# Performance work log

Hardware: AMD Instinct MI355X
Metric: run time of the kernel (lower is better)

## Reference

```python
import jax, jax.numpy as jnp
import numpy as np

DEPTH = 18                      # perfect binary tree depth -> N = 2**DEPTH - 1 nodes
N_NODES = 2 ** DEPTH - 1        # 262143
VOCAB, E, H = 2048, 64, 64


def setup_inputs() -> dict:
    key = jax.random.key(0)
    ks = jax.random.split(key, 10)
    token_ids = jax.random.randint(ks[0], (N_NODES,), 0, VOCAB, dtype=jnp.int32)
    emb = jax.random.normal(ks[1], (VOCAB, E), dtype=jnp.float32)
    emb = emb.at[0].set(0.0)  # padding_idx=0 row is zero in torch
    s = 0.1  # keep gates out of hard saturation
    return {
        "token_ids": token_ids,
        "emb": emb,
        "W_iou": jax.random.normal(ks[2], (3 * H, E), dtype=jnp.float32) * s,
        "b_Wiou": jnp.zeros((3 * H,), dtype=jnp.float32),
        "U_iou": jax.random.normal(ks[3], (3 * H, 2 * H), dtype=jnp.float32) * s,
        "b_Uiou": jnp.zeros((3 * H,), dtype=jnp.float32),
        "W_f": jax.random.normal(ks[4], (2 * H, E), dtype=jnp.float32) * s,
        "b_Wf": jnp.zeros((2 * H,), dtype=jnp.float32),
        "U_f": jax.random.normal(ks[5], (2 * H, 2 * H), dtype=jnp.float32) * s,
        "b_Uf": jnp.zeros((2 * H,), dtype=jnp.float32),
        "depth": DEPTH,
    }


def _tree_lstm(token_ids, emb, W_iou, b_Wiou, U_iou, b_Uiou, W_f, b_Wf, U_f, b_Uf, depth):
    """Level-synchronous bottom-up Binary TreeLSTM over a perfect binary tree.

    Node i has children 2i+1 (left), 2i+2 (right); level l occupies
    indices [2**l - 1, 2**(l+1) - 2]. Children of level-l node k sit at
    offsets 2k, 2k+1 of level l+1, so a reshape gives (left, right) pairs.
    """
    Hd = W_f.shape[0] // 2
    h = c = None
    for l in range(depth - 1, -1, -1):
        start, n = 2 ** l - 1, 2 ** l
        x = emb[token_ids[start:start + n]]                    # [n, E]
        if h is None:  # leaves: zero left/right states (both children zero)
            h_cat = jnp.zeros((n, 2 * Hd), dtype=x.dtype)
            c_lr = jnp.zeros((n, 2, Hd), dtype=x.dtype)
        else:
            h_cat = h.reshape(n, 2 * Hd)                        # [h_l | h_r]
            c_lr = c.reshape(n, 2, Hd)
        iou = jax.nn.sigmoid(x @ W_iou.T + b_Wiou + h_cat @ U_iou.T + b_Uiou)
        i_g, o_g, u_g = jnp.split(iou, 3, axis=1)
        u_g = jnp.tanh(u_g)  # faithful: tanh(sigmoid(u_pre)) as in the source
        f = jax.nn.sigmoid(x @ W_f.T + b_Wf + h_cat @ U_f.T + b_Uf)
        f_l, f_r = f[:, :Hd], f[:, Hd:]
        c = i_g * u_g + f_l * c_lr[:, 0] + f_r * c_lr[:, 1]
        h = o_g * jnp.tanh(c)
    return jnp.stack([h, c])  # [2, 1, H]: root (h, c)


def reference(token_ids, emb, W_iou, b_Wiou, U_iou, b_Uiou, W_f, b_Wf, U_f, b_Uf, depth):
    return _tree_lstm(token_ids, emb, W_iou, b_Wiou, U_iou, b_Uiou,
                      W_f, b_Wf, U_f, b_Uf, depth)
```

## Files before the change

kernel.cpp:

```cpp
#include <hip/hip_runtime.h>

typedef __bf16 bf16;
typedef __bf16 bf16x8 __attribute__((ext_vector_type(8)));
typedef float f32x4 __attribute__((ext_vector_type(4)));

#define DEPTH   18
#define N_NODES ((1 << DEPTH) - 1)
#define KDIM    192
#define RDIM    320
#define A_PAD   200
#define LOG2E   1.4426950408889634f

__device__ __forceinline__ float rcpf(float x) { return __builtin_amdgcn_rcpf(x); }
__device__ __forceinline__ float sig2(float p)  { return rcpf(1.f + exp2f(-p)); }
__device__ __forceinline__ float tanhf_(float x){ return 2.f * rcpf(1.f + exp2f(-2.f * LOG2E * x)) - 1.f; }

__device__ __forceinline__ void gates(const f32x4* acc,
        const float4& bI, const float4& bO, const float4& bU,
        const float4& bL, const float4& bR,
        const float4& cl, const float4& cr, float4& c4, float4& h4) {
    const float* pbI = &bI.x; const float* pbO = &bO.x; const float* pbU = &bU.x;
    const float* pbL = &bL.x; const float* pbR = &bR.x;
    const float* pcl = &cl.x; const float* pcr = &cr.x;
    float* pc4 = &c4.x; float* ph4 = &h4.x;
#pragma unroll
    for (int r = 0; r < 4; r++) {
        float i_g = sig2(acc[0][r] + pbI[r]);
        float o_g = sig2(acc[1][r] + pbO[r]);
        float u_g = tanhf_(sig2(acc[2][r] + pbU[r]));
        float fl  = sig2(acc[3][r] + pbL[r]);
        float fr  = sig2(acc[4][r] + pbR[r]);
        float c = i_g * u_g + fl * pcl[r] + fr * pcr[r];
        pc4[r] = c;
        ph4[r] = o_g * tanhf_(c);
    }
}

__global__ void prep_all(const float* __restrict__ emb,
                     const float* __restrict__ W_iou, const float* __restrict__ U_iou,
                     const float* __restrict__ W_f,   const float* __restrict__ U_f,
                     const float* __restrict__ b_Wiou, const float* __restrict__ b_Uiou,
                     const float* __restrict__ b_Wf,   const float* __restrict__ b_Uf,
                     bf16* __restrict__ Wcat, float* __restrict__ bias, bf16* __restrict__ emb16,
                     bf16* __restrict__ leafH, float* __restrict__ leafC) {
    __shared__ __align__(16) bf16 Wl[192 * 72];
    __shared__ __align__(16) bf16 Al[64 * 72];
    const int blk = blockIdx.x, tid = threadIdx.x;
    if (blk < 512) {
        int t = blk * 256 + tid;
        emb16[t] = (bf16)emb[t];
        if (t < RDIM * KDIM) {
            int r = t / KDIM, k = t % KDIM;
            float v;
            if (r < 192) v = (k < 64) ? W_iou[r * 64 + k] : U_iou[r * 128 + (k - 64)];
            else { int rr = r - 192; v = (k < 64) ? W_f[rr * 64 + k] : U_f[rr * 128 + (k - 64)]; }
            Wcat[t] = (bf16)(v * LOG2E);
        }
        if (t < RDIM)
            bias[t] = ((t < 192) ? (b_Wiou[t] + b_Uiou[t]) : (b_Wf[t - 192] + b_Uf[t - 192])) * LOG2E;
        return;
    }
    const int v0 = (blk - 512) * 64;
    for (int i = tid; i < 192 * 64; i += 256) {
        int r = i >> 6, k = i & 63;
        Wl[r * 72 + k] = (bf16)(W_iou[i] * LOG2E);
    }
    for (int i = tid; i < 64 * 64; i += 256) {
        int r = i >> 6, k = i & 63;
        Al[r * 72 + k] = (bf16)emb[(v0 << 6) + i];
    }
    __syncthreads();
    const int wave = tid >> 6, lane = tid & 63;
    const int l15 = lane & 15, quad = lane >> 4;
    const int jw = (wave & 3) * 16, jb = jw + quad * 4;

    f32x4 acc[4][3];
#pragma unroll
    for (int t = 0; t < 4; t++)
#pragma unroll
        for (int g = 0; g < 3; g++) acc[t][g] = (f32x4){0.f, 0.f, 0.f, 0.f};
#pragma unroll
    for (int kb = 0; kb < 2; kb++) {
        bf16x8 wfrag[3], nfrag[4];
#pragma unroll
        for (int g = 0; g < 3; g++)
            wfrag[g] = *(const bf16x8*)(&Wl[(g * 64 + jw + l15) * 72 + kb * 32 + quad * 8]);
#pragma unroll
        for (int t = 0; t < 4; t++)
            nfrag[t] = *(const bf16x8*)(&Al[(t * 16 + l15) * 72 + kb * 32 + quad * 8]);
#pragma unroll
        for (int t = 0; t < 4; t++)
#pragma unroll
            for (int g = 0; g < 3; g++)
                acc[t][g] = __builtin_amdgcn_mfma_f32_16x16x32_bf16(wfrag[g], nfrag[t], acc[t][g], 0, 0, 0);
    }
    float4 bW, bU_;
    bW = *(const float4*)(b_Wiou + jb);       bU_ = *(const float4*)(b_Uiou + jb);
    float4 bI = make_float4((bW.x + bU_.x) * LOG2E, (bW.y + bU_.y) * LOG2E, (bW.z + bU_.z) * LOG2E, (bW.w + bU_.w) * LOG2E);
    bW = *(const float4*)(b_Wiou + 64 + jb);  bU_ = *(const float4*)(b_Uiou + 64 + jb);
    float4 bO = make_float4((bW.x + bU_.x) * LOG2E, (bW.y + bU_.y) * LOG2E, (bW.z + bU_.z) * LOG2E, (bW.w + bU_.w) * LOG2E);
    bW = *(const float4*)(b_Wiou + 128 + jb); bU_ = *(const float4*)(b_Uiou + 128 + jb);
    float4 bU = make_float4((bW.x + bU_.x) * LOG2E, (bW.y + bU_.y) * LOG2E, (bW.z + bU_.z) * LOG2E, (bW.w + bU_.w) * LOG2E);
    const float* pbI = &bI.x; const float* pbO = &bO.x; const float* pbU = &bU.x;
#pragma unroll
    for (int t = 0; t < 4; t++) {
        int v = v0 + t * 16 + l15;
        float4 c4; float* pc4 = &c4.x;
        union { bf16 h[4]; uint2 u; } hp;
#pragma unroll
        for (int r = 0; r < 4; r++) {
            float i_g = sig2(acc[t][0][r] + pbI[r]);
            float o_g = sig2(acc[t][1][r] + pbO[r]);
            float u_g = tanhf_(sig2(acc[t][2][r] + pbU[r]));
            float c = i_g * u_g;
            pc4[r] = c;
            hp.h[r] = (bf16)(o_g * tanhf_(c));
        }
        *(float4*)(leafC + (size_t)v * 64 + jb) = c4;
        *(uint2*)(leafH + (size_t)v * 64 + jb) = hp.u;
    }
}

template<int NQ, bool CGLOB>
__device__ __forceinline__ void level_phase(
        int l, int blk, int tid, int wt, int l15, int quad, int jb,
        const bf16x8 (&Wf)[5][6],
        const float4& bI, const float4& bO, const float4& bU,
        const float4& bL, const float4& bR,
        bf16* Acur, bf16* Anx,
        const bf16* __restrict__ emb16, const int* __restrict__ token_ids,
        bf16* __restrict__ H, float* __restrict__ c_buf)
{
    const int m = 1 << (l - 8);
    const int s = (1 << l) - 1, o = blk * m;
    const int T = (m + 15) >> 4;
    const int mn = m >> 1;
    const float* Cin = (const float*)(Acur + m * A_PAD);

    float4 pcl[NQ], pcr[NQ];
    int pidx[NQ], pgn[NQ]; bool pact[NQ];
#pragma unroll
    for (int q = 0; q < NQ; q++) {
        int ti = wt + 2 * q;
        int idx0 = ti * 16 + l15;
        bool act = (ti < T) && (idx0 < m);
        int idx = act ? idx0 : 0;
        pidx[q] = idx; pact[q] = act; pgn[q] = s + o + idx;
        if (CGLOB) {
            pcl[q] = *(const float4*)(c_buf + (size_t)(2 * pgn[q] + 1) * 64 + jb);
            pcr[q] = *(const float4*)(c_buf + (size_t)(2 * pgn[q] + 2) * 64 + jb);
        } else {
            pcl[q] = *(const float4*)(Cin + (2 * idx) * 68 + jb);
            pcr[q] = *(const float4*)(Cin + (2 * idx + 1) * 68 + jb);
        }
    }

    int tok = 0;
    const int srow = tid >> 3, sk8 = (tid & 7) << 3;
    const bool sact = (l > 8) && (tid < mn * 8);
    if (sact) tok = token_ids[(1 << (l - 1)) - 1 + blk * mn + srow];

    float* Cout = (float*)(Anx + mn * A_PAD);
#pragma unroll
    for (int q = 0; q < NQ; q++) {
        f32x4 acc[5];
#pragma unroll
        for (int g = 0; g < 5; g++) acc[g] = (f32x4){0.f, 0.f, 0.f, 0.f};
#pragma unroll
        for (int kb = 0; kb < 6; kb++) {
            bf16x8 nf = *(const bf16x8*)(&Acur[pidx[q] * A_PAD + kb * 32 + quad * 8]);
#pragma unroll
            for (int g = 0; g < 5; g++)
                acc[g] = __builtin_amdgcn_mfma_f32_16x16x32_bf16(Wf[g][kb], nf, acc[g], 0, 0, 0);
        }
        float4 c4, h4;
        gates(acc, bI, bO, bU, bL, bR, pcl[q], pcr[q], c4, h4);
        if (pact[q]) {
            union { bf16 h[4]; uint2 u; } hp;
            const float* ph4 = &h4.x;
#pragma unroll
            for (int r = 0; r < 4; r++) hp.h[r] = (bf16)ph4[r];
            if (l > 8) {
                *(float4*)(Cout + pidx[q] * 68 + jb) = c4;
                *(uint2*)(&Anx[(pidx[q] >> 1) * A_PAD + 64 + (pidx[q] & 1) * 64 + jb]) = hp.u;
            } else {
                *(float4*)(c_buf + (size_t)pgn[q] * 64 + jb) = c4;
                *(uint2*)(H + (size_t)pgn[q] * 64 + jb) = hp.u;
            }
        }
    }

    if (sact) {
        uint4 g = *(const uint4*)(emb16 + (size_t)tok * 64 + sk8);
        *(uint4*)(&Anx[srow * A_PAD + sk8]) = g;
    }
    __syncthreads();
}

__global__ __launch_bounds__(512, 1) void big_pass(
        const bf16* __restrict__ Wcat, const float* __restrict__ bias,
        const bf16* __restrict__ emb16, const int* __restrict__ token_ids,
        const bf16* __restrict__ leafH, const float* __restrict__ leafC,
        bf16* __restrict__ H, float* __restrict__ c_buf) {
    __shared__ __align__(16) bf16 A0[256 * A_PAD];
    __shared__ __align__(16) bf16 A1[128 * A_PAD];
    const int tid = threadIdx.x, blk = blockIdx.x;
    const int wave = tid >> 6, lane = tid & 63;
    const int l15 = lane & 15, quad = lane >> 4;
    const int wj = wave & 3, wt = wave >> 2;
    const int jw = wj * 16, jb = jw + quad * 4;

    const int base16 = 65535 + blk * 256;

    for (int ch = tid; ch < 256 * 8; ch += 512) {
        int row = ch >> 3, k8 = (ch & 7) << 3;
        int tok = token_ids[base16 + row];
        *(uint4*)&A0[row * A_PAD + k8] = *(const uint4*)(emb16 + tok * 64 + k8);
    }
    for (int ch = tid; ch < 256 * 16; ch += 512) {
        int row = ch >> 4, half = (ch >> 3) & 1, k8 = (ch & 7) << 3;
        int tok = token_ids[2 * (base16 + row) + 1 + half];
        *(uint4*)&A0[row * A_PAD + 64 + half * 64 + k8] = *(const uint4*)(leafH + (size_t)tok * 64 + k8);
    }

    int tkl16[8], tkr16[8];
#pragma unroll
    for (int q = 0; q < 8; q++) {
        int idx = (wt + 2 * q) * 16 + l15;
        int gn = base16 + idx;
        tkl16[q] = token_ids[2 * gn + 1];
        tkr16[q] = token_ids[2 * gn + 2];
    }
    const int rowa = tid >> 3, k8a = (tid & 7) << 3;
    const int rowb = (tid + 512) >> 3, k8b = k8a;
    const int tok15a = token_ids[32767 + blk * 128 + rowa];
    const int tok15b = token_ids[32767 + blk * 128 + rowb];

    bf16x8 Wf[5][6];
#pragma unroll
    for (int g = 0; g < 5; g++)
#pragma unroll
        for (int kb = 0; kb < 6; kb++)
            Wf[g][kb] = *(const bf16x8*)(Wcat + (g * 64 + jw + l15) * KDIM + kb * 32 + quad * 8);

    const float4 bI = *(const float4*)(bias + jb);
    const float4 bO = *(const float4*)(bias + 64 + jb);
    const float4 bU = *(const float4*)(bias + 128 + jb);
    const float4 bL = *(const float4*)(bias + 192 + jb);
    const float4 bR = *(const float4*)(bias + 256 + jb);
    __syncthreads();

#pragma unroll
    for (int grp = 0; grp < 2; grp++) {
        float4 cl4[4], cr4[4];
#pragma unroll
        for (int q = 0; q < 4; q++) {
            cl4[q] = *(const float4*)(leafC + (size_t)tkl16[grp * 4 + q] * 64 + jb);
            cr4[q] = *(const float4*)(leafC + (size_t)tkr16[grp * 4 + q] * 64 + jb);
        }
#pragma unroll
        for (int q = 0; q < 4; q++) {
            const int idx = (wt + 2 * (grp * 4 + q)) * 16 + l15;
            const int gn = base16 + idx;
            f32x4 acc[5];
#pragma unroll
            for (int g = 0; g < 5; g++) acc[g] = (f32x4){0.f, 0.f, 0.f, 0.f};
#pragma unroll
            for (int kb = 0; kb < 6; kb++) {
                bf16x8 nf = *(const bf16x8*)(&A0[idx * A_PAD + kb * 32 + quad * 8]);
#pragma unroll
                for (int g = 0; g < 5; g++)
                    acc[g] = __builtin_amdgcn_mfma_f32_16x16x32_bf16(Wf[g][kb], nf, acc[g], 0, 0, 0);
            }
            float4 c4, h4;
            gates(acc, bI, bO, bU, bL, bR, cl4[q], cr4[q], c4, h4);
            union { bf16 h[4]; uint2 u; } hp;
            const float* ph4 = &h4.x;
#pragma unroll
            for (int r = 0; r < 4; r++) hp.h[r] = (bf16)ph4[r];
            *(float4*)(c_buf + (size_t)gn * 64 + jb) = c4;
            *(uint2*)(&A1[(idx >> 1) * A_PAD + 64 + (idx & 1) * 64 + jb]) = hp.u;
        }
        if (grp == 0) {
            uint4 ga = *(const uint4*)(emb16 + (size_t)tok15a * 64 + k8a);
            uint4 gb = *(const uint4*)(emb16 + (size_t)tok15b * 64 + k8b);
            *(uint4*)(&A1[rowa * A_PAD + k8a]) = ga;
            *(uint4*)(&A1[rowb * A_PAD + k8b]) = gb;
        }
    }
    __syncthreads();

    bf16* Acur = A1;
    bf16* Anx  = A0;
    level_phase<4, true >(15, blk, tid, wt, l15, quad, jb, Wf, bI, bO, bU, bL, bR,
                          Acur, Anx, emb16, token_ids, H, c_buf);
    { bf16* t = Acur; Acur = Anx; Anx = t; }
    level_phase<2, false>(14, blk, tid, wt, l15, quad, jb, Wf, bI, bO, bU, bL, bR,
                          Acur, Anx, emb16, token_ids, H, c_buf);
    { bf16* t = Acur; Acur = Anx; Anx = t; }
    for (int l = 13; l >= 8; l--) {
        level_phase<1, false>(l, blk, tid, wt, l15, quad, jb, Wf, bI, bO, bU, bL, bR,
                              Acur, Anx, emb16, token_ids, H, c_buf);
        bf16* t = Acur; Acur = Anx; Anx = t;
    }
}

__global__ __launch_bounds__(512) void tail_pass(
        const bf16* __restrict__ Wcat, const float* __restrict__ bias,
        const bf16* __restrict__ emb16, const int* __restrict__ token_ids,
        const bf16* __restrict__ H, const float* __restrict__ c_buf,
        float* __restrict__ out) {
    __shared__ __align__(16) bf16 A[255 * A_PAD];
    __shared__ __align__(16) float C0[128 * 68];
    __shared__ __align__(16) float C1[64 * 68];
    const int tid = threadIdx.x;
    const int wave = tid >> 6, lane = tid & 63;
    const int l15 = lane & 15, quad = lane >> 4;
    const int wj = wave & 3, wt = wave >> 2;
    const int jw = wj * 16, jb = jw + quad * 4;

    float4 cl7[4], cr7[4];
#pragma unroll
    for (int q = 0; q < 4; q++) {
        int idx = (wt + 2 * q) * 16 + l15;
        int gn = 127 + idx;
        cl7[q] = *(const float4*)(c_buf + (size_t)(2 * gn + 1) * 64 + jb);
        cr7[q] = *(const float4*)(c_buf + (size_t)(2 * gn + 2) * 64 + jb);
    }

    for (int ch = tid; ch < 255 * 8; ch += 512) {
        int row = ch >> 3, k8 = (ch & 7) << 3;
        int l = 31 - __clz(255 - row);
        int idx = row - 256 + (2 << l);
        int gn = (1 << l) - 1 + idx;
        int tok = token_ids[gn];
        *(uint4*)&A[row * A_PAD + k8] = *(const uint4*)(emb16 + tok * 64 + k8);
    }
    for (int ch = tid; ch < 128 * 16; ch += 512) {
        int row = ch >> 4, k8 = (ch & 15) << 3;
        *(uint4*)&A[row * A_PAD + 64 + k8] =
            *(const uint4*)(H + (size_t)(255 + 2 * row) * 64 + k8);
    }

    bf16x8 Wf[5][6];
#pragma unroll
    for (int g = 0; g < 5; g++)
#pragma unroll
        for (int kb = 0; kb < 6; kb++)
            Wf[g][kb] = *(const bf16x8*)(Wcat + (g * 64 + jw + l15) * KDIM + kb * 32 + quad * 8);

    const float4 bI = *(const float4*)(bias + jb);
    const float4 bO = *(const float4*)(bias + 64 + jb);
    const float4 bU = *(const float4*)(bias + 128 + jb);
    const float4 bL = *(const float4*)(bias + 192 + jb);
    const float4 bR = *(const float4*)(bias + 256 + jb);
    __syncthreads();

#pragma unroll
    for (int q = 0; q < 4; q++) {
        const int idx = (wt + 2 * q) * 16 + l15;
        f32x4 acc[5];
#pragma unroll
        for (int g = 0; g < 5; g++) acc[g] = (f32x4){0.f, 0.f, 0.f, 0.f};
#pragma unroll
        for (int kb = 0; kb < 6; kb++) {
            bf16x8 nf = *(const bf16x8*)(&A[idx * A_PAD + kb * 32 + quad * 8]);
#pragma unroll
            for (int g = 0; g < 5; g++)
                acc[g] = __builtin_amdgcn_mfma_f32_16x16x32_bf16(Wf[g][kb], nf, acc[g], 0, 0, 0);
        }
        float4 c4, h4;
        gates(acc, bI, bO, bU, bL, bR, cl7[q], cr7[q], c4, h4);
        union { bf16 h[4]; uint2 u; } hp;
        const float* ph4 = &h4.x;
#pragma unroll
        for (int r = 0; r < 4; r++) hp.h[r] = (bf16)ph4[r];
        *(float4*)(C0 + idx * 68 + jb) = c4;
        *(uint2*)(&A[(128 + (idx >> 1)) * A_PAD + 64 + (idx & 1) * 64 + jb]) = hp.u;
    }
    __syncthreads();

    float* Ccur = C0;
    float* Cnx  = C1;
    for (int l = 6; l >= 0; l--) {
        const int n = 1 << l;
        const int off  = 256 - 2 * n;
        const int offn = 256 - n;
        const int T = (n + 15) >> 4;
        for (int ti = wt; ti < T; ti += 2) {
            int idx0 = ti * 16 + l15;
            int idx = idx0 < n ? idx0 : n - 1;
            float4 cl = *(const float4*)(Ccur + (2 * idx) * 68 + jb);
            float4 cr = *(const float4*)(Ccur + (2 * idx + 1) * 68 + jb);
            f32x4 acc[5];
#pragma unroll
            for (int g = 0; g < 5; g++) acc[g] = (f32x4){0.f, 0.f, 0.f, 0.f};
#pragma unroll
            for (int kb = 0; kb < 6; kb++) {
                bf16x8 nf = *(const bf16x8*)(&A[(off + idx) * A_PAD + kb * 32 + quad * 8]);
#pragma unroll
                for (int g = 0; g < 5; g++)
                    acc[g] = __builtin_amdgcn_mfma_f32_16x16x32_bf16(Wf[g][kb], nf, acc[g], 0, 0, 0);
            }
            float4 c4, h4;
            gates(acc, bI, bO, bU, bL, bR, cl, cr, c4, h4);
            if (idx0 < n) {
                if (l > 0) {
                    union { bf16 h[4]; uint2 u; } hp;
                    const float* ph4 = &h4.x;
#pragma unroll
                    for (int r = 0; r < 4; r++) hp.h[r] = (bf16)ph4[r];
                    *(float4*)(Cnx + idx * 68 + jb) = c4;
                    *(uint2*)(&A[(offn + (idx >> 1)) * A_PAD + 64 + (idx & 1) * 64 + jb]) = hp.u;
                } else {
                    *(float4*)(out + jb) = h4;
                    *(float4*)(out + 64 + jb) = c4;
                }
            }
        }
        __syncthreads();
        float* t = Ccur; Ccur = Cnx; Cnx = t;
    }
}

extern "C" void kernel_launch(void* const* d_in, const int* in_sizes, int n_in,
                              void* d_out, int out_size, void* d_ws, size_t ws_size,
                              hipStream_t stream) {
    const int*   token_ids = (const int*)d_in[0];
    const float* emb       = (const float*)d_in[1];
    const float* W_iou     = (const float*)d_in[2];
    const float* b_Wiou    = (const float*)d_in[3];
    const float* U_iou     = (const float*)d_in[4];
    const float* b_Uiou    = (const float*)d_in[5];
    const float* W_f       = (const float*)d_in[6];
    const float* b_Wf      = (const float*)d_in[7];
    const float* U_f       = (const float*)d_in[8];
    const float* b_Uf      = (const float*)d_in[9];
    float* out = (float*)d_out;

    char* ws = (char*)d_ws;
    bf16*  Wcat  = (bf16*)ws;
    float* bias  = (float*)(ws + 122880);
    bf16*  emb16 = (bf16*)(ws + 124160);
    bf16*  leafH = (bf16*)(ws + 386304);
    float* leafC = (float*)(ws + 648448);
    bf16*  H     = (bf16*)(ws + 1172736);
    float* c_buf = (float*)(ws + 1238272);

    prep_all<<<544, 256, 0, stream>>>(emb, W_iou, U_iou, W_f, U_f,
                                      b_Wiou, b_Uiou, b_Wf, b_Uf,
                                      Wcat, bias, emb16, leafH, leafC);
    big_pass<<<256, 512, 0, stream>>>(Wcat, bias, emb16, token_ids, leafH, leafC, H, c_buf);
    tail_pass<<<1, 512, 0, stream>>>(Wcat, bias, emb16, token_ids, H, c_buf, out);
}
```

Baseline: 162.1 us.

## Fuse tail pass into big pass via last-block atomic counter

Merges the single-block tail kernel into the 256-block big pass. Each block increments a global counter after its subtree, and the last block to finish runs the top levels. Shared memory is unioned into one buffer that both phases reuse. This removes one kernel launch and the gap between launches, at the cost of an atomic, memory fences, and a counter that prep_all must reset.

```diff
diff --git a/kernel.cpp b/kernel.cpp
--- a/kernel.cpp
+++ b/kernel.cpp
@@ -42,10 +42,12 @@
                      const float* __restrict__ b_Wiou, const float* __restrict__ b_Uiou,
                      const float* __restrict__ b_Wf,   const float* __restrict__ b_Uf,
                      bf16* __restrict__ Wcat, float* __restrict__ bias, bf16* __restrict__ emb16,
-                     bf16* __restrict__ leafH, float* __restrict__ leafC) {
+                     bf16* __restrict__ leafH, float* __restrict__ leafC,
+                     int* __restrict__ done_cnt) {
     __shared__ __align__(16) bf16 Wl[192 * 72];
     __shared__ __align__(16) bf16 Al[64 * 72];
     const int blk = blockIdx.x, tid = threadIdx.x;
+    if (blk == 0 && tid == 0) *done_cnt = 0;
     if (blk < 512) {
         int t = blk * 256 + tid;
         emb16[t] = (bf16)emb[t];
@@ -197,229 +199,234 @@
     __syncthreads();
 }
 
-__global__ __launch_bounds__(512, 1) void big_pass(
+__global__ __launch_bounds__(512, 1) void big_tail(
         const bf16* __restrict__ Wcat, const float* __restrict__ bias,
         const bf16* __restrict__ emb16, const int* __restrict__ token_ids,
         const bf16* __restrict__ leafH, const float* __restrict__ leafC,
-        bf16* __restrict__ H, float* __restrict__ c_buf) {
-    __shared__ __align__(16) bf16 A0[256 * A_PAD];
-    __shared__ __align__(16) bf16 A1[128 * A_PAD];
+        bf16* __restrict__ H, float* __restrict__ c_buf,
+        int* __restrict__ done_cnt, float* __restrict__ out) {
+    __shared__ __align__(16) char smem[154224];
+    __shared__ int is_last;
     const int tid = threadIdx.x, blk = blockIdx.x;
     const int wave = tid >> 6, lane = tid & 63;
     const int l15 = lane & 15, quad = lane >> 4;
     const int wj = wave & 3, wt = wave >> 2;
     const int jw = wj * 16, jb = jw + quad * 4;
 
-    const int base16 = 65535 + blk * 256;
-
-    for (int ch = tid; ch < 256 * 8; ch += 512) {
-        int row = ch >> 3, k8 = (ch & 7) << 3;
-        int tok = token_ids[base16 + row];
-        *(uint4*)&A0[row * A_PAD + k8] = *(const uint4*)(emb16 + tok * 64 + k8);
-    }
-    for (int ch = tid; ch < 256 * 16; ch += 512) {
-        int row = ch >> 4, half = (ch >> 3) & 1, k8 = (ch & 7) << 3;
-        int tok = token_ids[2 * (base16 + row) + 1 + half];
-        *(uint4*)&A0[row * A_PAD + 64 + half * 64 + k8] = *(const uint4*)(leafH + (size_t)tok * 64 + k8);
-    }
-
-    int tkl16[8], tkr16[8];
-#pragma unroll
-    for (int q = 0; q < 8; q++) {
-        int idx = (wt + 2 * q) * 16 + l15;
-        int gn = base16 + idx;
-        tkl16[q] = token_ids[2 * gn + 1];
-        tkr16[q] = token_ids[2 * gn + 2];
-    }
-    const int rowa = tid >> 3, k8a = (tid & 7) << 3;
-    const int rowb = (tid + 512) >> 3, k8b = k8a;
-    const int tok15a = token_ids[32767 + blk * 128 + rowa];
-    const int tok15b = token_ids[32767 + blk * 128 + rowb];
-
-    bf16x8 Wf[5][6];
-#pragma unroll
-    for (int g = 0; g < 5; g++)
-#pragma unroll
-        for (int kb = 0; kb < 6; kb++)
-            Wf[g][kb] = *(const bf16x8*)(Wcat + (g * 64 + jw + l15) * KDIM + kb * 32 + quad * 8);
-
-    const float4 bI = *(const float4*)(bias + jb);
-    const float4 bO = *(const float4*)(bias + 64 + jb);
-    const float4 bU = *(const float4*)(bias + 128 + jb);
-    const float4 bL = *(const float4*)(bias + 192 + jb);
-    const float4 bR = *(const float4*)(bias + 256 + jb);
+    {
+        bf16* A0 = (bf16*)smem;
+        bf16* A1 = (bf16*)(smem + 102400);
+        const int base16 = 65535 + blk * 256;
+
+        for (int ch = tid; ch < 256 * 8; ch += 512) {
+            int row = ch >> 3, k8 = (ch & 7) << 3;
+            int tok = token_ids[base16 + row];
+            *(uint4*)&A0[row * A_PAD + k8] = *(const uint4*)(emb16 + tok * 64 + k8);
+        }
+        for (int ch = tid; ch < 256 * 16; ch += 512) {
+            int row = ch >> 4, half = (ch >> 3) & 1, k8 = (ch & 7) << 3;
+            int tok = token_ids[2 * (base16 + row) + 1 + half];
+            *(uint4*)&A0[row * A_PAD + 64 + half * 64 + k8] = *(const uint4*)(leafH + (size_t)tok * 64 + k8);
+        }
+
+        int tkl16[8], tkr16[8];
+#pragma unroll
+        for (int q = 0; q < 8; q++) {
+            int idx = (wt + 2 * q) * 16 + l15;
+            int gn = base16 + idx;
+            tkl16[q] = token_ids[2 * gn + 1];
+            tkr16[q] = token_ids[2 * gn + 2];
+        }
+        const int rowa = tid >> 3, k8a = (tid & 7) << 3;
+        const int rowb = (tid + 512) >> 3, k8b = k8a;
+        const int tok15a = token_ids[32767 + blk * 128 + rowa];
+        const int tok15b = token_ids[32767 + blk * 128 + rowb];
+
+        bf16x8 Wf[5][6];
+#pragma unroll
+        for (int g = 0; g < 5; g++)
+#pragma unroll
+            for (int kb = 0; kb < 6; kb++)
+                Wf[g][kb] = *(const bf16x8*)(Wcat + (g * 64 + jw + l15) * KDIM + kb * 32 + quad * 8);
+
+        const float4 bI = *(const float4*)(bias + jb);
+        const float4 bO = *(const float4*)(bias + 64 + jb);
+        const float4 bU = *(const float4*)(bias + 128 + jb);
+        const float4 bL = *(const float4*)(bias + 192 + jb);
+        const float4 bR = *(const float4*)(bias + 256 + jb);
+        __syncthreads();
+
+#pragma unroll
+        for (int grp = 0; grp < 2; grp++) {
+            float4 cl4[4], cr4[4];
+#pragma unroll
+            for (int q = 0; q < 4; q++) {
+                cl4[q] = *(const float4*)(leafC + (size_t)tkl16[grp * 4 + q] * 64 + jb);
+                cr4[q] = *(const float4*)(leafC + (size_t)tkr16[grp * 4 + q] * 64 + jb);
+            }
+#pragma unroll
+            for (int q = 0; q < 4; q++) {
+                const int idx = (wt + 2 * (grp * 4 + q)) * 16 + l15;
+                const int gn = base16 + idx;
+                f32x4 acc[5];
+#pragma unroll
+                for (int g = 0; g < 5; g++) acc[g] = (f32x4){0.f, 0.f, 0.f, 0.f};
+#pragma unroll
+                for (int kb = 0; kb < 6; kb++) {
+                    bf16x8 nf = *(const bf16x8*)(&A0[idx * A_PAD + kb * 32 + quad * 8]);
+#pragma unroll
+                    for (int g = 0; g < 5; g++)
+                        acc[g] = __builtin_amdgcn_mfma_f32_16x16x32_bf16(Wf[g][kb], nf, acc[g], 0, 0, 0);
+                }
+                float4 c4, h4;
+                gates(acc, bI, bO, bU, bL, bR, cl4[q], cr4[q], c4, h4);
+                union { bf16 h[4]; uint2 u; } hp;
+                const float* ph4 = &h4.x;
+#pragma unroll
+                for (int r = 0; r < 4; r++) hp.h[r] = (bf16)ph4[r];
+                *(float4*)(c_buf + (size_t)gn * 64 + jb) = c4;
+                *(uint2*)(&A1[(idx >> 1) * A_PAD + 64 + (idx & 1) * 64 + jb]) = hp.u;
+            }
+            if (grp == 0) {
+                uint4 ga = *(const uint4*)(emb16 + (size_t)tok15a * 64 + k8a);
+                uint4 gb = *(const uint4*)(emb16 + (size_t)tok15b * 64 + k8b);
+                *(uint4*)(&A1[rowa * A_PAD + k8a]) = ga;
+                *(uint4*)(&A1[rowb * A_PAD + k8b]) = gb;
+            }
+        }
+        __syncthreads();
+
+        bf16* Acur = A1;
+        bf16* Anx  = A0;
+        level_phase<4, true >(15, blk, tid, wt, l15, quad, jb, Wf, bI, bO, bU, bL, bR,
+                              Acur, Anx, emb16, token_ids, H, c_buf);
+        { bf16* t = Acur; Acur = Anx; Anx = t; }
+        level_phase<2, false>(14, blk, tid, wt, l15, quad, jb, Wf, bI, bO, bU, bL, bR,
+                              Acur, Anx, emb16, token_ids, H, c_buf);
+        { bf16* t = Acur; Acur = Anx; Anx = t; }
+        for (int l = 13; l >= 8; l--) {
+            level_phase<1, false>(l, blk, tid, wt, l15, quad, jb, Wf, bI, bO, bU, bL, bR,
+                                  Acur, Anx, emb16, token_ids, H, c_buf);
+            bf16* t = Acur; Acur = Anx; Anx = t;
+        }
+    }
+
+    if (tid == 0) {
+        __threadfence();
+        int old = atomicAdd(done_cnt, 1);
+        is_last = (old == 255);
+    }
     __syncthreads();
-
-#pragma unroll
-    for (int grp = 0; grp < 2; grp++) {
-        float4 cl4[4], cr4[4];
+    if (!is_last) return;
+    __threadfence();
+
+    {
+        bf16*  A  = (bf16*)smem;
+        float* C0 = (float*)(smem + 102000);
+        float* C1 = (float*)(smem + 136816);
+
+        float4 cl7[4], cr7[4];
 #pragma unroll
         for (int q = 0; q < 4; q++) {
-            cl4[q] = *(const float4*)(leafC + (size_t)tkl16[grp * 4 + q] * 64 + jb);
-            cr4[q] = *(const float4*)(leafC + (size_t)tkr16[grp * 4 + q] * 64 + jb);
-        }
+            int idx = (wt + 2 * q) * 16 + l15;
+            int gn = 127 + idx;
+            cl7[q] = *(const float4*)(c_buf + (size_t)(2 * gn + 1) * 64 + jb);
+            cr7[q] = *(const float4*)(c_buf + (size_t)(2 * gn + 2) * 64 + jb);
+        }
+
+        for (int ch = tid; ch < 255 * 8; ch += 512) {
+            int row = ch >> 3, k8 = (ch & 7) << 3;
+            int l = 31 - __clz(255 - row);
+            int idx = row - 256 + (2 << l);
+            int gn = (1 << l) - 1 + idx;
+            int tok = token_ids[gn];
+            *(uint4*)&A[row * A_PAD + k8] = *(const uint4*)(emb16 + tok * 64 + k8);
+        }
+        for (int ch = tid; ch < 128 * 16; ch += 512) {
+            int row = ch >> 4, k8 = (ch & 15) << 3;
+            *(uint4*)&A[row * A_PAD + 64 + k8] =
+                *(const uint4*)(H + (size_t)(255 + 2 * row) * 64 + k8);
+        }
+
+        bf16x8 Wf[5][6];
+#pragma unroll
+        for (int g = 0; g < 5; g++)
+#pragma unroll
+            for (int kb = 0; kb < 6; kb++)
+                Wf[g][kb] = *(const bf16x8*)(Wcat + (g * 64 + jw + l15) * KDIM + kb * 32 + quad * 8);
+
+        const float4 bI = *(const float4*)(bias + jb);
+        const float4 bO = *(const float4*)(bias + 64 + jb);
+        const float4 bU = *(const float4*)(bias + 128 + jb);
+        const float4 bL = *(const float4*)(bias + 192 + jb);
+        const float4 bR = *(const float4*)(bias + 256 + jb);
+        __syncthreads();
+
 #pragma unroll
         for (int q = 0; q < 4; q++) {
-            const int idx = (wt + 2 * (grp * 4 + q)) * 16 + l15;
-            const int gn = base16 + idx;
+            const int idx = (wt + 2 * q) * 16 + l15;
             f32x4 acc[5];
 #pragma unroll
             for (int g = 0; g < 5; g++) acc[g] = (f32x4){0.f, 0.f, 0.f, 0.f};
 #pragma unroll
             for (int kb = 0; kb < 6; kb++) {
-                bf16x8 nf = *(const bf16x8*)(&A0[idx * A_PAD + kb * 32 + quad * 8]);
+                bf16x8 nf = *(const bf16x8*)(&A[idx * A_PAD + kb * 32 + quad * 8]);
 #pragma unroll
                 for (int g = 0; g < 5; g++)
                     acc[g] = __builtin_amdgcn_mfma_f32_16x16x32_bf16(Wf[g][kb], nf, acc[g], 0, 0, 0);
             }
             float4 c4, h4;
-            gates(acc, bI, bO, bU, bL, bR, cl4[q], cr4[q], c4, h4);
+            gates(acc, bI, bO, bU, bL, bR, cl7[q], cr7[q], c4, h4);
             union { bf16 h[4]; uint2 u; } hp;
             const float* ph4 = &h4.x;
 #pragma unroll
             for (int r = 0; r < 4; r++) hp.h[r] = (bf16)ph4[r];
-            *(float4*)(c_buf + (size_t)gn * 64 + jb) = c4;
-            *(uint2*)(&A1[(idx >> 1) * A_PAD + 64 + (idx & 1) * 64 + jb]) = hp.u;
-        }
-        if (grp == 0) {
-            uint4 ga = *(const uint4*)(emb16 + (size_t)tok15a * 64 + k8a);
-            uint4 gb = *(const uint4*)(emb16 + (size_t)tok15b * 64 + k8b);
-            *(uint4*)(&A1[rowa * A_PAD + k8a]) = ga;
-            *(uint4*)(&A1[rowb * A_PAD + k8b]) = gb;
-        }
-    }
-    __syncthreads();
-
-    bf16* Acur = A1;
-    bf16* Anx  = A0;
-    level_phase<4, true >(15, blk, tid, wt, l15, quad, jb, Wf, bI, bO, bU, bL, bR,
-                          Acur, Anx, emb16, token_ids, H, c_buf);
-    { bf16* t = Acur; Acur = Anx; Anx = t; }
-    level_phase<2, false>(14, blk, tid, wt, l15, quad, jb, Wf, bI, bO, bU, bL, bR,
-                          Acur, Anx, emb16, token_ids, H, c_buf);
-    { bf16* t = Acur; Acur = Anx; Anx = t; }
-    for (int l = 13; l >= 8; l--) {
-        level_phase<1, false>(l, blk, tid, wt, l15, quad, jb, Wf, bI, bO, bU, bL, bR,
-                              Acur, Anx, emb16, token_ids, H, c_buf);
-        bf16* t = Acur; Acur = Anx; Anx = t;
-    }
-}
-
-__global__ __launch_bounds__(512) void tail_pass(
-        const bf16* __restrict__ Wcat, const float* __restrict__ bias,
-        const bf16* __restrict__ emb16, const int* __restrict__ token_ids,
-        const bf16* __restrict__ H, const float* __restrict__ c_buf,
-        float* __restrict__ out) {
-    __shared__ __align__(16) bf16 A[255 * A_PAD];
-    __shared__ __align__(16) float C0[128 * 68];
-    __shared__ __align__(16) float C1[64 * 68];
-    const int tid = threadIdx.x;
-    const int wave = tid >> 6, lane = tid & 63;
-    const int l15 = lane & 15, quad = lane >> 4;
-    const int wj = wave & 3, wt = wave >> 2;
-    const int jw = wj * 16, jb = jw + quad * 4;
-
-    float4 cl7[4], cr7[4];
-#pragma unroll
-    for (int q = 0; q < 4; q++) {
-        int idx = (wt + 2 * q) * 16 + l15;
-        int gn = 127 + idx;
-        cl7[q] = *(const float4*)(c_buf + (size_t)(2 * gn + 1) * 64 + jb);
-        cr7[q] = *(const float4*)(c_buf + (size_t)(2 * gn + 2) * 64 + jb);
-    }
-
-    for (int ch = tid; ch < 255 * 8; ch += 512) {
-        int row = ch >> 3, k8 = (ch & 7) << 3;
-        int l = 31 - __clz(255 - row);
-        int idx = row - 256 + (2 << l);
-        int gn = (1 << l) - 1 + idx;
-        int tok = token_ids[gn];
-        *(uint4*)&A[row * A_PAD + k8] = *(const uint4*)(emb16 + tok * 64 + k8);
-    }
-    for (int ch = tid; ch < 128 * 16; ch += 512) {
-        int row = ch >> 4, k8 = (ch & 15) << 3;
-        *(uint4*)&A[row * A_PAD + 64 + k8] =
-            *(const uint4*)(H + (size_t)(255 + 2 * row) * 64 + k8);
-    }
-
-    bf16x8 Wf[5][6];
-#pragma unroll
-    for (int g = 0; g < 5; g++)
-#pragma unroll
-        for (int kb = 0; kb < 6; kb++)
-            Wf[g][kb] = *(const bf16x8*)(Wcat + (g * 64 + jw + l15) * KDIM + kb * 32 + quad * 8);
-
-    const float4 bI = *(const float4*)(bias + jb);
-    const float4 bO = *(const float4*)(bias + 64 + jb);
-    const float4 bU = *(const float4*)(bias + 128 + jb);
-    const float4 bL = *(const float4*)(bias + 192 + jb);
-    const float4 bR = *(const float4*)(bias + 256 + jb);
-    __syncthreads();
-
-#pragma unroll
-    for (int q = 0; q < 4; q++) {
-        const int idx = (wt + 2 * q) * 16 + l15;
-        f32x4 acc[5];
-#pragma unroll
-        for (int g = 0; g < 5; g++) acc[g] = (f32x4){0.f, 0.f, 0.f, 0.f};
-#pragma unroll
-        for (int kb = 0; kb < 6; kb++) {
-            bf16x8 nf = *(const bf16x8*)(&A[idx * A_PAD + kb * 32 + quad * 8]);
-#pragma unroll
-            for (int g = 0; g < 5; g++)
-                acc[g] = __builtin_amdgcn_mfma_f32_16x16x32_bf16(Wf[g][kb], nf, acc[g], 0, 0, 0);
-        }
-        float4 c4, h4;
-        gates(acc, bI, bO, bU, bL, bR, cl7[q], cr7[q], c4, h4);
-        union { bf16 h[4]; uint2 u; } hp;
-        const float* ph4 = &h4.x;
-#pragma unroll
-        for (int r = 0; r < 4; r++) hp.h[r] = (bf16)ph4[r];
-        *(float4*)(C0 + idx * 68 + jb) = c4;
-        *(uint2*)(&A[(128 + (idx >> 1)) * A_PAD + 64 + (idx & 1) * 64 + jb]) = hp.u;
-    }
-    __syncthreads();
-
-    float* Ccur = C0;
-    float* Cnx  = C1;
-    for (int l = 6; l >= 0; l--) {
-        const int n = 1 << l;
-        const int off  = 256 - 2 * n;
-        const int offn = 256 - n;
-        const int T = (n + 15) >> 4;
-        for (int ti = wt; ti < T; ti += 2) {
-            int idx0 = ti * 16 + l15;
-            int idx = idx0 < n ? idx0 : n - 1;
-            float4 cl = *(const float4*)(Ccur + (2 * idx) * 68 + jb);
-            float4 cr = *(const float4*)(Ccur + (2 * idx + 1) * 68 + jb);
-            f32x4 acc[5];
-#pragma unroll
-            for (int g = 0; g < 5; g++) acc[g] = (f32x4){0.f, 0.f, 0.f, 0.f};
-#pragma unroll
-            for (int kb = 0; kb < 6; kb++) {
-                bf16x8 nf = *(const bf16x8*)(&A[(off + idx) * A_PAD + kb * 32 + quad * 8]);
-#pragma unroll
-                for (int g = 0; g < 5; g++)
-                    acc[g] = __builtin_amdgcn_mfma_f32_16x16x32_bf16(Wf[g][kb], nf, acc[g], 0, 0, 0);
-            }
-            float4 c4, h4;
-            gates(acc, bI, bO, bU, bL, bR, cl, cr, c4, h4);
-            if (idx0 < n) {
-                if (l > 0) {
-                    union { bf16 h[4]; uint2 u; } hp;
-                    const float* ph4 = &h4.x;
-#pragma unroll
-                    for (int r = 0; r < 4; r++) hp.h[r] = (bf16)ph4[r];
-                    *(float4*)(Cnx + idx * 68 + jb) = c4;
-                    *(uint2*)(&A[(offn + (idx >> 1)) * A_PAD + 64 + (idx & 1) * 64 + jb]) = hp.u;
-                } else {
-                    *(float4*)(out + jb) = h4;
-                    *(float4*)(out + 64 + jb) = c4;
+            *(float4*)(C0 + idx * 68 + jb) = c4;
+            *(uint2*)(&A[(128 + (idx >> 1)) * A_PAD + 64 + (idx & 1) * 64 + jb]) = hp.u;
+        }
+        __syncthreads();
+
+        float* Ccur = C0;
+        float* Cnx  = C1;
+        for (int l = 6; l >= 0; l--) {
+            const int n = 1 << l;
+            const int off  = 256 - 2 * n;
+            const int offn = 256 - n;
+            const int T = (n + 15) >> 4;
+            for (int ti = wt; ti < T; ti += 2) {
+                int idx0 = ti * 16 + l15;
+                int idx = idx0 < n ? idx0 : n - 1;
+                float4 cl = *(const float4*)(Ccur + (2 * idx) * 68 + jb);
+                float4 cr = *(const float4*)(Ccur + (2 * idx + 1) * 68 + jb);
+                f32x4 acc[5];
+#pragma unroll
+                for (int g = 0; g < 5; g++) acc[g] = (f32x4){0.f, 0.f, 0.f, 0.f};
+#pragma unroll
+                for (int kb = 0; kb < 6; kb++) {
+                    bf16x8 nf = *(const bf16x8*)(&A[(off + idx) * A_PAD + kb * 32 + quad * 8]);
+#pragma unroll
+                    for (int g = 0; g < 5; g++)
+                        acc[g] = __builtin_amdgcn_mfma_f32_16x16x32_bf16(Wf[g][kb], nf, acc[g], 0, 0, 0);
                 }
-            }
-        }
-        __syncthreads();
-        float* t = Ccur; Ccur = Cnx; Cnx = t;
+                float4 c4, h4;
+                gates(acc, bI, bO, bU, bL, bR, cl, cr, c4, h4);
+                if (idx0 < n) {
+                    if (l > 0) {
+                        union { bf16 h[4]; uint2 u; } hp;
+                        const float* ph4 = &h4.x;
+#pragma unroll
+                        for (int r = 0; r < 4; r++) hp.h[r] = (bf16)ph4[r];
+                        *(float4*)(Cnx + idx * 68 + jb) = c4;
+                        *(uint2*)(&A[(offn + (idx >> 1)) * A_PAD + 64 + (idx & 1) * 64 + jb]) = hp.u;
+                    } else {
+                        *(float4*)(out + jb) = h4;
+                        *(float4*)(out + 64 + jb) = c4;
+                    }
+                }
+            }
+            __syncthreads();
+            float* t = Ccur; Ccur = Cnx; Cnx = t;
+        }
     }
 }
 
@@ -446,10 +453,11 @@
     float* leafC = (float*)(ws + 648448);
     bf16*  H     = (bf16*)(ws + 1172736);
     float* c_buf = (float*)(ws + 1238272);
+    int*   done_cnt = (int*)(ws + 34792704);
 
     prep_all<<<544, 256, 0, stream>>>(emb, W_iou, U_iou, W_f, U_f,
                                       b_Wiou, b_Uiou, b_Wf, b_Uf,
-                                      Wcat, bias, emb16, leafH, leafC);
-    big_pass<<<256, 512, 0, stream>>>(Wcat, bias, emb16, token_ids, leafH, leafC, H, c_buf);
-    tail_pass<<<1, 512, 0, stream>>>(Wcat, bias, emb16, token_ids, H, c_buf, out);
+                                      Wcat, bias, emb16, leafH, leafC, done_cnt);
+    big_tail<<<256, 512, 0, stream>>>(Wcat, bias, emb16, token_ids, leafH, leafC,
+                                      H, c_buf, done_cnt, out);
 }
```

Result: slower. 169.3 us (+4.4%).
